# Optimization experiments

Measured on AMD Instinct MI355X. Metric: run time of the kernel, lower is better.

Reference implementation:

```python
import jax, jax.numpy as jnp
import numpy as np
import itertools


def _comb_indices(F, k):
    # Flattened combination indices: for each of C(F,k) combinations, its k
    # member feature ids, concatenated. Row i of the original one-hot crmatrix
    # has a single 1 at column idx[i], so x @ crmatrix^T == gather by idx.
    return np.fromiter(itertools.chain(*itertools.combinations(range(F), k)),
                       dtype=np.int32)


def setup_inputs() -> dict:
    key = jax.random.key(0)
    x = jax.random.normal(key, (32, 4096, 32), dtype=jnp.float32)  # [B, T, F]
    return {"x": x, "k": 2}


def reference(x, k):
    F = x.shape[2]
    idx = jnp.asarray(_comb_indices(F, k))          # [ncr] = [k * C(F,k)]
    # Faithful to K.dot(x, crmatrix) with one-hot crmatrix: a feature gather.
    return jnp.take(x, idx, axis=2)                 # [B, T, ncr]
```

## Files before the change

### kernel.cpp

```cpp
#include <hip/hip_runtime.h>


#define FDIM 32
#define NCR 992
#define G_PER_ROW 248
#define BLOCK 256
#define GRID 2048

typedef float f32x4 __attribute__((ext_vector_type(4)));

__global__ __launch_bounds__(BLOCK, 8)
void comb_gather_kernel(const float* __restrict__ x,
                        float* __restrict__ out,
                        int nrows) {
    const unsigned total   = (unsigned)nrows * G_PER_ROW;
    const unsigned nthread = GRID * BLOCK;
    unsigned G = blockIdx.x * BLOCK + threadIdx.x;

    f32x4* outv = reinterpret_cast<f32x4*>(out);

    #pragma unroll 4
    for (; G < total; G += nthread) {
        const unsigned row = G / G_PER_ROW;
        const unsigned g   = G - row * G_PER_ROW;

        const int c0 = 2 * (int)g;
        float s = sqrtf(3969.0f - 8.0f * (float)c0);
        int i0 = (int)((63.0f - s) * 0.5f);
        if (i0 < 0) i0 = 0;
        int st0  = (i0 * (63 - i0)) >> 1;
        int stn0 = ((i0 + 1) * (62 - i0)) >> 1;
        if (stn0 <= c0) { i0++; st0 = stn0; stn0 = ((i0 + 1) * (62 - i0)) >> 1; }
        else if (st0 > c0) { i0--; stn0 = st0; st0 = (i0 * (63 - i0)) >> 1; }
        const int f0 = i0;
        const int f1 = c0 - st0 + i0 + 1;
        const int c1 = c0 + 1;
        int i1 = i0, st1 = st0;
        if (stn0 <= c1) { i1 = i0 + 1; st1 = stn0; }
        const int f2 = i1;
        const int f3 = c1 - st1 + i1 + 1;

        const float* rowp = x + (size_t)row * FDIM;
        f32x4 v;
        v.x = rowp[f0];
        v.y = rowp[f1];
        v.z = rowp[f2];
        v.w = rowp[f3];

        __builtin_nontemporal_store(v, outv + G);
    }
}

extern "C" void kernel_launch(void* const* d_in, const int* in_sizes, int n_in,
                              void* d_out, int out_size, void* d_ws, size_t ws_size,
                              hipStream_t stream) {
    const float* x  = (const float*)d_in[0];
    float* out      = (float*)d_out;
    int nrows = in_sizes[0] / FDIM;
    hipLaunchKernelGGL(comb_gather_kernel, dim3(GRID), dim3(BLOCK), 0, stream,
                       x, out, nrows);
}
```

Measured before the change: 104.5 us.

## Precompute packed feature indices in LDS and use per-wave contiguous unrolled chunks

Computes the packed four-feature index for each of the 248 groups once per block into shared memory, replacing the per-element sqrt-based combination decode with an LDS lookup. The grid shrinks to 256 blocks and each wave now handles contiguous chunks of 8x64 vector stores per iteration, with a fast path that skips bounds checks. The launch-bounds occupancy hint is dropped and the nontemporal stores become plain stores. The aim is to cut ALU overhead and raise memory-level parallelism, at the cost of fewer resident waves and possible cache pollution from ordinary stores on a write-heavy kernel.

```diff
diff --git a/kernel.cpp b/kernel.cpp
--- a/kernel.cpp
+++ b/kernel.cpp
@@ -5,26 +5,21 @@
 #define NCR 992
 #define G_PER_ROW 248
 #define BLOCK 256
-#define GRID 2048
+#define GRID 256
+#define UNROLL 8
 
 typedef float f32x4 __attribute__((ext_vector_type(4)));
 
-__global__ __launch_bounds__(BLOCK, 8)
+__global__ __launch_bounds__(BLOCK)
 void comb_gather_kernel(const float* __restrict__ x,
                         float* __restrict__ out,
                         int nrows) {
-    const unsigned total   = (unsigned)nrows * G_PER_ROW;
-    const unsigned nthread = GRID * BLOCK;
-    unsigned G = blockIdx.x * BLOCK + threadIdx.x;
+    __shared__ int featp[G_PER_ROW];
 
-    f32x4* outv = reinterpret_cast<f32x4*>(out);
+    const int tid = threadIdx.x;
 
-    #pragma unroll 4
-    for (; G < total; G += nthread) {
-        const unsigned row = G / G_PER_ROW;
-        const unsigned g   = G - row * G_PER_ROW;
-
-        const int c0 = 2 * (int)g;
+    if (tid < G_PER_ROW) {
+        const int c0 = 2 * tid;
         float s = sqrtf(3969.0f - 8.0f * (float)c0);
         int i0 = (int)((63.0f - s) * 0.5f);
         if (i0 < 0) i0 = 0;
@@ -39,15 +34,55 @@
         if (stn0 <= c1) { i1 = i0 + 1; st1 = stn0; }
         const int f2 = i1;
         const int f3 = c1 - st1 + i1 + 1;
+        featp[tid] = f0 | (f1 << 8) | (f2 << 16) | (f3 << 24);
+    }
+    __syncthreads();
 
-        const float* rowp = x + (size_t)row * FDIM;
-        f32x4 v;
-        v.x = rowp[f0];
-        v.y = rowp[f1];
-        v.z = rowp[f2];
-        v.w = rowp[f3];
+    const unsigned T    = (unsigned)nrows * G_PER_ROW;
+    const unsigned gtid = blockIdx.x * BLOCK + tid;
+    const unsigned wave = gtid >> 6;
+    const unsigned lane = gtid & 63;
+    const unsigned nw   = (GRID * BLOCK) >> 6;
+    const unsigned wstep = UNROLL * 64;
+    const unsigned step  = nw * wstep;
 
-        __builtin_nontemporal_store(v, outv + G);
+    f32x4* outv = reinterpret_cast<f32x4*>(out);
+    const unsigned G0 = wave * wstep + lane;
+
+    for (unsigned base = G0; base < T; base += step) {
+        if (base + (UNROLL - 1) * 64 < T) {
+            #pragma unroll
+            for (int u = 0; u < UNROLL; ++u) {
+                const unsigned G   = base + u * 64;
+                const unsigned row = G / G_PER_ROW;
+                const unsigned g   = G - row * G_PER_ROW;
+                const int p = featp[g];
+                const float* rowp = x + (size_t)row * FDIM;
+                f32x4 v;
+                v.x = rowp[p & 0xff];
+                v.y = rowp[(p >> 8) & 0xff];
+                v.z = rowp[(p >> 16) & 0xff];
+                v.w = rowp[(p >> 24) & 0xff];
+                outv[G] = v;
+            }
+        } else {
+            #pragma unroll
+            for (int u = 0; u < UNROLL; ++u) {
+                const unsigned G = base + u * 64;
+                if (G < T) {
+                    const unsigned row = G / G_PER_ROW;
+                    const unsigned g   = G - row * G_PER_ROW;
+                    const int p = featp[g];
+                    const float* rowp = x + (size_t)row * FDIM;
+                    f32x4 v;
+                    v.x = rowp[p & 0xff];
+                    v.y = rowp[(p >> 8) & 0xff];
+                    v.z = rowp[(p >> 16) & 0xff];
+                    v.w = rowp[(p >> 24) & 0xff];
+                    outv[G] = v;
+                }
+            }
+        }
     }
 }
 
```

After: 180.3 us. 1.73x slower.
